# Kernel optimization log

Measured on AMD Instinct MI355X. Metric: run time of the kernel, lower is better.

Reference implementation:

```python
import jax, jax.numpy as jnp
import numpy as np

NFPS = 10

def setup_inputs() -> dict:
    key = jax.random.key(0)
    k1, k2, k3, k4 = jax.random.split(key, 4)
    B, D_IN, H, D_OUT = 131072, 2 * NFPS * 3, 256, NFPS * 3 * 12
    x = jax.random.normal(k1, (B, D_IN), dtype=jnp.float32)
    centres = jax.random.normal(k2, (H, D_IN), dtype=jnp.float32)
    sigmas = jax.random.uniform(k3, (H,), dtype=jnp.float32)
    W2 = jax.random.normal(k4, (D_OUT, H), dtype=jnp.float32) * (1.0 / np.sqrt(H))
    return {"x": x, "centres": centres, "sigmas": sigmas, "W2": W2}

def reference(x, centres, sigmas, W2):
    # RBF layer: distances = ||x - c|| * sigma; gaussian: exp(-distances^2)
    x2 = jnp.sum(x * x, axis=-1, keepdims=True)            # [B,1]
    c2 = jnp.sum(centres * centres, axis=-1)               # [H]
    xc = jnp.einsum('bd,hd->bh', x, centres)               # [B,H]
    d2 = jnp.maximum(x2 + c2[None, :] - 2.0 * xc, 0.0)     # squared distance, clamp fp noise
    phi = jnp.exp(-(sigmas[None, :] ** 2) * d2)            # [B,H]
    out = jnp.einsum('bh,oh->bo', phi, W2)                 # [B, nFPs*3*12]
    B = x.shape[0]
    out = out.reshape(B, NFPS, 12, 3).transpose(0, 1, 3, 2).reshape(B, 3 * NFPS, 12)
    return out
```

## Files before the change

kernel.cpp:

```cpp
#include <hip/hip_runtime.h>

#define THREADS 512
#define DIN 60
#define HN 256
#define DOUT 360

typedef __attribute__((ext_vector_type(8))) short short8;
typedef __attribute__((ext_vector_type(4))) float f32x4;
typedef __attribute__((ext_vector_type(2))) float f32x2;
typedef __attribute__((ext_vector_type(4))) unsigned int u32x4;

#define WS_CBF   0
#define WS_CN    32768
#define WS_W2    34816

__device__ __forceinline__ short bf16_bits(float f) {
    union { float f; unsigned u; } v; v.f = f;
    unsigned r = (v.u + 0x7FFFu + ((v.u >> 16) & 1u)) >> 16;
    return (short)(unsigned short)r;
}

__device__ __forceinline__ unsigned pk_bf16(float a, float b) {
    unsigned r;
    asm("v_cvt_pk_bf16_f32 %0, %1, %2" : "=v"(r) : "v"(a), "v"(b));
    return r;
}

__device__ __forceinline__ void gload16(const void* g, void* lds) {
    __builtin_amdgcn_global_load_lds(
        (const __attribute__((address_space(1))) unsigned int*)(uintptr_t)g,
        (__attribute__((address_space(3))) unsigned int*)(unsigned int)(uintptr_t)lds,
        16, 0, 0);
}

__global__ void prep(const float* __restrict__ centres, const float* __restrict__ sigmas,
                     const float* __restrict__ W2, short* __restrict__ ws)
{
    int t = blockIdx.x * 256 + threadIdx.x;
    if (t < 12288) {
        int row = t >> 5, pc = t & 31;
        int c = pc ^ (row & 7);
        short8 v = {0,0,0,0,0,0,0,0};
        if (row < DOUT) {
            int rr = row / 12, jj = row % 12;
            int f = rr / 3, kk = rr % 3;
            int o = f * 36 + jj * 3 + kk;
            const float* src = W2 + o * HN + c * 8;
            #pragma unroll
            for (int i = 0; i < 8; ++i) v[i] = bf16_bits(src[i]);
        }
        *(short8*)(ws + (WS_W2 / 2) + t * 8) = v;
    } else if (t < 14336) {
        int j = t - 12288;
        int row = j >> 3, p = j & 7;
        int c = p ^ (row & 7);
        short8 v = {0,0,0,0,0,0,0,0};
        #pragma unroll
        for (int i = 0; i < 8; ++i) {
            int k = c * 8 + i;
            if (k < DIN) v[i] = bf16_bits(centres[row * DIN + k]);
        }
        *(short8*)(ws + (WS_CBF / 2) + j * 8) = v;
    } else if (t < 14592) {
        int i = t - 14336;
        const float* cr = centres + i * DIN;
        float s = 0.f;
        #pragma unroll
        for (int d = 0; d < DIN; ++d) s = fmaf(cr[d], cr[d], s);
        float sg = sigmas[i];
        float ns2 = -sg * sg * 1.44269504088896340736f;
        f32x2 v; v[0] = ns2; v[1] = ns2 * s;
        *(f32x2*)(ws + (WS_CN / 2) + i * 4) = v;
    }
}

__global__ __launch_bounds__(THREADS, 2)
void rbf_main(const float* __restrict__ x, const short* __restrict__ ws,
              float* __restrict__ out)
{
    __shared__ short8 w2h[6144];
    __shared__ short8 cbf[2048];
    __shared__ f32x2  cnsl[HN];

    const int tid   = threadIdx.x;
    const int w     = tid >> 6;
    const int l15   = tid & 15;
    const int g     = (tid & 63) >> 4;
    const int f     = blockIdx.x & 1;
    const int sbase = blockIdx.x >> 1;

    #pragma unroll
    for (int i = 0; i < 12; ++i)
        gload16(ws + (WS_W2 / 2) + ((size_t)f * 6144 + i * THREADS + tid) * 8,
                (char*)w2h + (i * THREADS + tid) * 16);
    #pragma unroll
    for (int i = 0; i < 4; ++i)
        gload16(ws + (WS_CBF / 2) + (i * THREADS + tid) * 8, (char*)cbf + (i * THREADS + tid) * 16);
    if (tid < 128)
        gload16(ws + (WS_CN / 2) + tid * 8, (char*)cnsl + tid * 16);

    int rbase = sbase * 128 + w * 16;
    f32x4 xa[2][2];
    {
        const float* xr = x + (size_t)(rbase + l15) * DIN;
        #pragma unroll
        for (int kt = 0; kt < 2; ++kt) {
            int k0 = kt * 32 + g * 8;
            xa[kt][0] = *(const f32x4*)(xr + k0);
            xa[kt][1] = (k0 + 4 < DIN) ? *(const f32x4*)(xr + k0 + 4) : (f32x4){0.f,0.f,0.f,0.f};
        }
    }

    __syncthreads();

    for (int it = 0; it < 8; ++it) {
        float p2 = 0.f;
        #pragma unroll
        for (int kt = 0; kt < 2; ++kt)
            #pragma unroll
            for (int h = 0; h < 2; ++h)
                #pragma unroll
                for (int i = 0; i < 4; ++i) p2 = fmaf(xa[kt][h][i], xa[kt][h][i], p2);
        p2 += __shfl_xor(p2, 16);
        p2 += __shfl_xor(p2, 32);
        const float x2v = p2;

        short8 xb[2];
        #pragma unroll
        for (int kt = 0; kt < 2; ++kt) {
            union { u32x4 u; short8 s; } a;
            a.u[0] = pk_bf16(xa[kt][0][0], xa[kt][0][1]);
            a.u[1] = pk_bf16(xa[kt][0][2], xa[kt][0][3]);
            a.u[2] = pk_bf16(xa[kt][1][0], xa[kt][1][1]);
            a.u[3] = pk_bf16(xa[kt][1][2], xa[kt][1][3]);
            xb[kt] = a.s;
        }

        if (it < 7) {
            const float* xr = x + (size_t)(rbase + 16384 + l15) * DIN;
            #pragma unroll
            for (int kt = 0; kt < 2; ++kt) {
                int k0 = kt * 32 + g * 8;
                xa[kt][0] = *(const f32x4*)(xr + k0);
                xa[kt][1] = (k0 + 4 < DIN) ? *(const f32x4*)(xr + k0 + 4) : (f32x4){0.f,0.f,0.f,0.f};
            }
        }

        f32x4 acc1[16];
        #pragma unroll
        for (int nt = 0; nt < 16; ++nt) acc1[nt] = (f32x4){0.f, 0.f, 0.f, 0.f};
        __builtin_amdgcn_s_setprio(1);
        #pragma unroll
        for (int nt = 0; nt < 16; ++nt) {
            int row = nt * 16 + l15;
            #pragma unroll
            for (int kt = 0; kt < 2; ++kt) {
                short8 cf = cbf[row * 8 + ((kt * 4 + g) ^ (row & 7))];
                acc1[nt] = __builtin_amdgcn_mfma_f32_16x16x32_bf16(cf, xb[kt], acc1[nt], 0, 0, 0);
            }
        }
        __builtin_amdgcn_s_setprio(0);

        unsigned pw[16][2];
        #pragma unroll
        for (int nt = 0; nt < 16; ++nt) {
            float ph[4];
            #pragma unroll
            for (int r = 0; r < 4; ++r) {
                f32x2 cn = cnsl[nt * 16 + g * 4 + r];
                float t  = fmaf(-2.f, acc1[nt][r], x2v);
                float ex = fminf(fmaf(cn[0], t, cn[1]), 0.f);
                ph[r] = exp2f(ex);
            }
            pw[nt][0] = pk_bf16(ph[0], ph[1]);
            pw[nt][1] = pk_bf16(ph[2], ph[3]);
        }

        f32x4 acc2[12];
        #pragma unroll
        for (int nt = 0; nt < 12; ++nt) acc2[nt] = (f32x4){0.f, 0.f, 0.f, 0.f};

        const int s0 = l15 + ((g & 1) << 5);
        const bool hi = (g >= 2);

        #pragma unroll
        for (int kt = 0; kt < 8; ++kt) {
            int A0 = __shfl((int)pw[2*kt][0],   s0);
            int A1 = __shfl((int)pw[2*kt][1],   s0);
            int C0 = __shfl((int)pw[2*kt+1][0], s0);
            int C1 = __shfl((int)pw[2*kt+1][1], s0);
            int B0 = __shfl((int)pw[2*kt][0],   s0 + 16);
            int B1 = __shfl((int)pw[2*kt][1],   s0 + 16);
            int D0 = __shfl((int)pw[2*kt+1][0], s0 + 16);
            int D1 = __shfl((int)pw[2*kt+1][1], s0 + 16);
            union { u32x4 u; short8 s; } afu;
            afu.u[0] = (unsigned)(hi ? C0 : A0);
            afu.u[1] = (unsigned)(hi ? C1 : A1);
            afu.u[2] = (unsigned)(hi ? D0 : B0);
            afu.u[3] = (unsigned)(hi ? D1 : B1);

            __builtin_amdgcn_s_setprio(1);
            #pragma unroll
            for (int nt = 0; nt < 12; ++nt) {
                int lrow = nt * 16 + l15;
                short8 bf = w2h[lrow * 32 + ((kt * 4 + g) ^ (lrow & 7))];
                acc2[nt] = __builtin_amdgcn_mfma_f32_16x16x32_bf16(afu.s, bf, acc2[nt], 0, 0, 0);
            }
            __builtin_amdgcn_s_setprio(0);
        }

        {
            const size_t orow = (size_t)rbase + g * 4;
            #pragma unroll
            for (int nt = 0; nt < 12; ++nt) {
                int col = f * 192 + nt * 16 + l15;
                if (col < DOUT) {
                    #pragma unroll
                    for (int r = 0; r < 4; ++r)
                        out[(orow + r) * DOUT + col] = acc2[nt][r];
                }
            }
        }

        rbase += 16384;
    }
}

extern "C" void kernel_launch(void* const* d_in, const int* in_sizes, int n_in,
                              void* d_out, int out_size, void* d_ws, size_t ws_size,
                              hipStream_t stream) {
    const float* x       = (const float*)d_in[0];
    const float* centres = (const float*)d_in[1];
    const float* sigmas  = (const float*)d_in[2];
    const float* W2      = (const float*)d_in[3];
    float* out = (float*)d_out;
    short* ws  = (short*)d_ws;
    prep<<<dim3(57), dim3(256), 0, stream>>>(centres, sigmas, W2, ws);
    rbf_main<<<dim3(256), dim3(THREADS), 0, stream>>>(x, ws, out);
}
```

Measured before the change: 72.51 us.

## Fold RBF bias into GEMM padding and split outputs into quarters

The sigma scaling, the ||c||^2 term and the ||x||^2 term are folded into the first bf16 MFMA by using the padded K columns 60-63. ||x||^2 is split into hi/lo bf16 parts and multiplied by -sigma^2 stored in the centre matrix, so the epilogue shrinks to a min and exp2 with no per-element constant loads. The output columns are split across four blocks instead of two, which halves W2 LDS use per block and doubles the grid to 512 blocks with a launch bound of 4 blocks per CU. The prefetch of the next x tile is dropped and the x loads and first GEMM are recomputed in each quarter block, so more x traffic and more redundant GEMM1 work are traded for occupancy, with some precision risk from the bf16 bias terms.

```diff
diff --git a/kernel.cpp b/kernel.cpp
--- a/kernel.cpp
+++ b/kernel.cpp
@@ -7,12 +7,10 @@
 
 typedef __attribute__((ext_vector_type(8))) short short8;
 typedef __attribute__((ext_vector_type(4))) float f32x4;
-typedef __attribute__((ext_vector_type(2))) float f32x2;
 typedef __attribute__((ext_vector_type(4))) unsigned int u32x4;
 
 #define WS_CBF   0
-#define WS_CN    32768
-#define WS_W2    34816
+#define WS_W2    32768
 
 __device__ __forceinline__ short bf16_bits(float f) {
     union { float f; unsigned u; } v; v.f = f;
@@ -43,8 +41,8 @@
         short8 v = {0,0,0,0,0,0,0,0};
         if (row < DOUT) {
             int rr = row / 12, jj = row % 12;
-            int f = rr / 3, kk = rr % 3;
-            int o = f * 36 + jj * 3 + kk;
+            int fcl = rr / 3, kk = rr % 3;
+            int o = fcl * 36 + jj * 3 + kk;
             const float* src = W2 + o * HN + c * 8;
             #pragma unroll
             for (int i = 0; i < 8; ++i) v[i] = bf16_bits(src[i]);
@@ -54,131 +52,136 @@
         int j = t - 12288;
         int row = j >> 3, p = j & 7;
         int c = p ^ (row & 7);
+        const float* cr = centres + row * DIN;
+        float sg = sigmas[row];
+        union { unsigned u; float f; } nq;
+        nq.u = ((unsigned)(unsigned short)bf16_bits(2.f * sg * sg * 1.44269504088896340736f)) << 16;
+        const float nsq = nq.f;
         short8 v = {0,0,0,0,0,0,0,0};
-        #pragma unroll
-        for (int i = 0; i < 8; ++i) {
-            int k = c * 8 + i;
-            if (k < DIN) v[i] = bf16_bits(centres[row * DIN + k]);
+        if (c < 7) {
+            #pragma unroll
+            for (int i = 0; i < 8; ++i) {
+                int k = c * 8 + i;
+                if (k < DIN) v[i] = bf16_bits(nsq * cr[k]);
+            }
+        } else {
+            #pragma unroll
+            for (int i = 0; i < 4; ++i) v[i] = bf16_bits(nsq * cr[56 + i]);
+            float c2 = 0.f;
+            #pragma unroll
+            for (int d = 0; d < DIN; ++d) c2 = fmaf(cr[d], cr[d], c2);
+            float T = -0.5f * nsq * c2;
+            union { unsigned u; float f; } th;
+            th.u = ((unsigned)(unsigned short)bf16_bits(T)) << 16;
+            v[4] = bf16_bits(th.f);
+            v[5] = bf16_bits(T - th.f);
+            v[6] = bf16_bits(-0.5f * nsq);
+            v[7] = v[6];
         }
         *(short8*)(ws + (WS_CBF / 2) + j * 8) = v;
-    } else if (t < 14592) {
-        int i = t - 14336;
-        const float* cr = centres + i * DIN;
-        float s = 0.f;
-        #pragma unroll
-        for (int d = 0; d < DIN; ++d) s = fmaf(cr[d], cr[d], s);
-        float sg = sigmas[i];
-        float ns2 = -sg * sg * 1.44269504088896340736f;
-        f32x2 v; v[0] = ns2; v[1] = ns2 * s;
-        *(f32x2*)(ws + (WS_CN / 2) + i * 4) = v;
-    }
-}
-
-__global__ __launch_bounds__(THREADS, 2)
+    }
+}
+
+__device__ __forceinline__ void load_xtile16(const float* __restrict__ x, int row0,
+                                             int l15, int g, short8 xb[2]) {
+    const float* xr = x + (size_t)(row0 + l15) * DIN;
+    f32x4 xa[2][2];
+    #pragma unroll
+    for (int kt = 0; kt < 2; ++kt) {
+        int k0 = kt * 32 + g * 8;
+        xa[kt][0] = *(const f32x4*)(xr + k0);
+        xa[kt][1] = (k0 + 4 < DIN) ? *(const f32x4*)(xr + k0 + 4) : (f32x4){0.f,0.f,0.f,0.f};
+    }
+    float p2 = 0.f;
+    #pragma unroll
+    for (int kt = 0; kt < 2; ++kt)
+        #pragma unroll
+        for (int h = 0; h < 2; ++h)
+            #pragma unroll
+            for (int i = 0; i < 4; ++i) p2 = fmaf(xa[kt][h][i], xa[kt][h][i], p2);
+    p2 += __shfl_xor(p2, 16);
+    p2 += __shfl_xor(p2, 32);
+    union { unsigned u; float f; } hb; hb.u = pk_bf16(p2, 0.f) << 16;
+    float x2lo = p2 - hb.f;
+    #pragma unroll
+    for (int kt = 0; kt < 2; ++kt) {
+        union { u32x4 u; short8 s; } a;
+        a.u[0] = pk_bf16(xa[kt][0][0], xa[kt][0][1]);
+        a.u[1] = pk_bf16(xa[kt][0][2], xa[kt][0][3]);
+        a.u[2] = pk_bf16(xa[kt][1][0], xa[kt][1][1]);
+        a.u[3] = pk_bf16(xa[kt][1][2], xa[kt][1][3]);
+        if (kt == 1 && g == 3) {
+            a.u[2] = 0x3F803F80u;
+            a.u[3] = pk_bf16(hb.f, x2lo);
+        }
+        xb[kt] = a.s;
+    }
+}
+
+__global__ __launch_bounds__(THREADS, 4)
 void rbf_main(const float* __restrict__ x, const short* __restrict__ ws,
               float* __restrict__ out)
 {
-    __shared__ short8 w2h[6144];
+    __shared__ short8 w2q[3072];
     __shared__ short8 cbf[2048];
-    __shared__ f32x2  cnsl[HN];
-
-    const int tid   = threadIdx.x;
-    const int w     = tid >> 6;
-    const int l15   = tid & 15;
-    const int g     = (tid & 63) >> 4;
-    const int f     = blockIdx.x & 1;
-    const int sbase = blockIdx.x >> 1;
-
-    #pragma unroll
-    for (int i = 0; i < 12; ++i)
-        gload16(ws + (WS_W2 / 2) + ((size_t)f * 6144 + i * THREADS + tid) * 8,
-                (char*)w2h + (i * THREADS + tid) * 16);
+
+    const int tid  = threadIdx.x;
+    const int w    = tid >> 6;
+    const int lane = tid & 63;
+    const int l15  = lane & 15;
+    const int g    = lane >> 4;
+    const int bid  = blockIdx.x;
+    const int q     = (bid >> 3) & 3;
+    const int sbase = (bid & 7) | ((bid >> 5) << 3);
+
+    #pragma unroll
+    for (int i = 0; i < 6; ++i)
+        gload16(ws + (WS_W2 / 2) + ((size_t)q * 3072 + i * THREADS + tid) * 8,
+                (char*)w2q + (i * THREADS + tid) * 16);
     #pragma unroll
     for (int i = 0; i < 4; ++i)
         gload16(ws + (WS_CBF / 2) + (i * THREADS + tid) * 8, (char*)cbf + (i * THREADS + tid) * 16);
-    if (tid < 128)
-        gload16(ws + (WS_CN / 2) + tid * 8, (char*)cnsl + tid * 16);
-
-    int rbase = sbase * 128 + w * 16;
-    f32x4 xa[2][2];
-    {
-        const float* xr = x + (size_t)(rbase + l15) * DIN;
-        #pragma unroll
-        for (int kt = 0; kt < 2; ++kt) {
-            int k0 = kt * 32 + g * 8;
-            xa[kt][0] = *(const f32x4*)(xr + k0);
-            xa[kt][1] = (k0 + 4 < DIN) ? *(const f32x4*)(xr + k0 + 4) : (f32x4){0.f,0.f,0.f,0.f};
-        }
-    }
 
     __syncthreads();
 
     for (int it = 0; it < 8; ++it) {
-        float p2 = 0.f;
-        #pragma unroll
-        for (int kt = 0; kt < 2; ++kt)
-            #pragma unroll
-            for (int h = 0; h < 2; ++h)
+        const int rbase = sbase * 1024 + it * 128 + w * 16;
+
+        short8 xb[2];
+        load_xtile16(x, rbase, l15, g, xb);
+
+        unsigned pw[16][2];
+        #pragma unroll
+        for (int h2 = 0; h2 < 2; ++h2) {
+            f32x4 acc1[8];
+            #pragma unroll
+            for (int nt = 0; nt < 8; ++nt) acc1[nt] = (f32x4){0.f, 0.f, 0.f, 0.f};
+            __builtin_amdgcn_s_setprio(1);
+            #pragma unroll
+            for (int nt = 0; nt < 8; ++nt) {
+                int row = (h2 * 8 + nt) * 16 + l15;
                 #pragma unroll
-                for (int i = 0; i < 4; ++i) p2 = fmaf(xa[kt][h][i], xa[kt][h][i], p2);
-        p2 += __shfl_xor(p2, 16);
-        p2 += __shfl_xor(p2, 32);
-        const float x2v = p2;
-
-        short8 xb[2];
-        #pragma unroll
-        for (int kt = 0; kt < 2; ++kt) {
-            union { u32x4 u; short8 s; } a;
-            a.u[0] = pk_bf16(xa[kt][0][0], xa[kt][0][1]);
-            a.u[1] = pk_bf16(xa[kt][0][2], xa[kt][0][3]);
-            a.u[2] = pk_bf16(xa[kt][1][0], xa[kt][1][1]);
-            a.u[3] = pk_bf16(xa[kt][1][2], xa[kt][1][3]);
-            xb[kt] = a.s;
-        }
-
-        if (it < 7) {
-            const float* xr = x + (size_t)(rbase + 16384 + l15) * DIN;
-            #pragma unroll
-            for (int kt = 0; kt < 2; ++kt) {
-                int k0 = kt * 32 + g * 8;
-                xa[kt][0] = *(const f32x4*)(xr + k0);
-                xa[kt][1] = (k0 + 4 < DIN) ? *(const f32x4*)(xr + k0 + 4) : (f32x4){0.f,0.f,0.f,0.f};
-            }
-        }
-
-        f32x4 acc1[16];
-        #pragma unroll
-        for (int nt = 0; nt < 16; ++nt) acc1[nt] = (f32x4){0.f, 0.f, 0.f, 0.f};
-        __builtin_amdgcn_s_setprio(1);
-        #pragma unroll
-        for (int nt = 0; nt < 16; ++nt) {
-            int row = nt * 16 + l15;
-            #pragma unroll
-            for (int kt = 0; kt < 2; ++kt) {
-                short8 cf = cbf[row * 8 + ((kt * 4 + g) ^ (row & 7))];
-                acc1[nt] = __builtin_amdgcn_mfma_f32_16x16x32_bf16(cf, xb[kt], acc1[nt], 0, 0, 0);
-            }
-        }
-        __builtin_amdgcn_s_setprio(0);
-
-        unsigned pw[16][2];
-        #pragma unroll
-        for (int nt = 0; nt < 16; ++nt) {
-            float ph[4];
-            #pragma unroll
-            for (int r = 0; r < 4; ++r) {
-                f32x2 cn = cnsl[nt * 16 + g * 4 + r];
-                float t  = fmaf(-2.f, acc1[nt][r], x2v);
-                float ex = fminf(fmaf(cn[0], t, cn[1]), 0.f);
-                ph[r] = exp2f(ex);
-            }
-            pw[nt][0] = pk_bf16(ph[0], ph[1]);
-            pw[nt][1] = pk_bf16(ph[2], ph[3]);
-        }
-
-        f32x4 acc2[12];
-        #pragma unroll
-        for (int nt = 0; nt < 12; ++nt) acc2[nt] = (f32x4){0.f, 0.f, 0.f, 0.f};
+                for (int kt = 0; kt < 2; ++kt) {
+                    short8 cf = cbf[row * 8 + ((kt * 4 + g) ^ (row & 7))];
+                    acc1[nt] = __builtin_amdgcn_mfma_f32_16x16x32_bf16(cf, xb[kt], acc1[nt], 0, 0, 0);
+                }
+            }
+            __builtin_amdgcn_s_setprio(0);
+            #pragma unroll
+            for (int nt = 0; nt < 8; ++nt) {
+                int ntg = h2 * 8 + nt;
+                float ph[4];
+                #pragma unroll
+                for (int r = 0; r < 4; ++r)
+                    ph[r] = exp2f(fminf(acc1[nt][r], 0.f));
+                pw[ntg][0] = pk_bf16(ph[0], ph[1]);
+                pw[ntg][1] = pk_bf16(ph[2], ph[3]);
+            }
+        }
+
+        f32x4 acc2[6];
+        #pragma unroll
+        for (int nt = 0; nt < 6; ++nt) acc2[nt] = (f32x4){0.f, 0.f, 0.f, 0.f};
 
         const int s0 = l15 + ((g & 1) << 5);
         const bool hi = (g >= 2);
@@ -201,28 +204,24 @@
 
             __builtin_amdgcn_s_setprio(1);
             #pragma unroll
-            for (int nt = 0; nt < 12; ++nt) {
+            for (int nt = 0; nt < 6; ++nt) {
                 int lrow = nt * 16 + l15;
-                short8 bf = w2h[lrow * 32 + ((kt * 4 + g) ^ (lrow & 7))];
+                short8 bf = w2q[lrow * 32 + ((kt * 4 + g) ^ (lrow & 7))];
                 acc2[nt] = __builtin_amdgcn_mfma_f32_16x16x32_bf16(afu.s, bf, acc2[nt], 0, 0, 0);
             }
             __builtin_amdgcn_s_setprio(0);
         }
 
-        {
-            const size_t orow = (size_t)rbase + g * 4;
-            #pragma unroll
-            for (int nt = 0; nt < 12; ++nt) {
-                int col = f * 192 + nt * 16 + l15;
-                if (col < DOUT) {
-                    #pragma unroll
-                    for (int r = 0; r < 4; ++r)
-                        out[(orow + r) * DOUT + col] = acc2[nt][r];
-                }
-            }
-        }
-
-        rbase += 16384;
+        const int orow = rbase + g * 4;
+        #pragma unroll
+        for (int nt = 0; nt < 6; ++nt) {
+            int col = q * 96 + nt * 16 + l15;
+            if (col < DOUT) {
+                #pragma unroll
+                for (int r = 0; r < 4; ++r)
+                    out[(size_t)(orow + r) * DOUT + col] = acc2[nt][r];
+            }
+        }
     }
 }
 
@@ -235,6 +234,6 @@
     const float* W2      = (const float*)d_in[3];
     float* out = (float*)d_out;
     short* ws  = (short*)d_ws;
-    prep<<<dim3(57), dim3(256), 0, stream>>>(centres, sigmas, W2, ws);
-    rbf_main<<<dim3(256), dim3(THREADS), 0, stream>>>(x, ws, out);
-}
+    prep<<<dim3(56), dim3(256), 0, stream>>>(centres, sigmas, W2, ws);
+    rbf_main<<<dim3(512), dim3(THREADS), 0, stream>>>(x, ws, out);
+}
```

After: 81.55 us. 1.12x slower.
